# Optimization experiments

Measured on AMD Instinct MI355X. Metric: run time of the kernel, lower is better.

## Reference

```python
import jax, jax.numpy as jnp
import numpy as np

DIM = 256
HEADS = 8
DIM_HEAD = 64
INNER = HEADS * DIM_HEAD  # 512
B, N = 4, 1024


def setup_inputs() -> dict:
    key = jax.random.key(0)
    ks = jax.random.split(key, 7)
    x = jax.random.normal(ks[0], (B, N, DIM), dtype=jnp.float32)
    attn_bias = jax.random.normal(ks[1], (B, HEADS, N, N), dtype=jnp.float32)
    s = 1.0 / np.sqrt(DIM)
    Wq = jax.random.normal(ks[2], (DIM, INNER), dtype=jnp.float32) * s
    Wkv = jax.random.normal(ks[3], (DIM, 2 * INNER), dtype=jnp.float32) * s
    # to_out initialized to zero in the torch module; use small random so output is non-trivial
    Wo = jax.random.normal(ks[4], (INNER, DIM), dtype=jnp.float32) * (1.0 / np.sqrt(INNER))
    bo = jnp.zeros((DIM,), dtype=jnp.float32)
    # gating initialized weight=0, bias=1 -> sigmoid(1); use small random weight + bias 1
    Wg = jax.random.normal(ks[5], (DIM, INNER), dtype=jnp.float32) * 0.02
    bg = jnp.ones((INNER,), dtype=jnp.float32)
    return {"x": x, "attn_bias": attn_bias, "Wq": Wq, "Wkv": Wkv,
            "Wo": Wo, "bo": bo, "Wg": Wg, "bg": bg}


def reference(x, attn_bias, Wq, Wkv, Wo, bo, Wg, bg):
    b, n, _ = x.shape
    scale = DIM_HEAD ** -0.5
    q = x @ Wq                                    # [b, n, inner]
    kv = x @ Wkv                                  # [b, n, 2*inner]
    k, v = jnp.split(kv, 2, axis=-1)
    def split_heads(t):
        return t.reshape(b, n, HEADS, DIM_HEAD).transpose(0, 2, 1, 3)  # [b,h,n,d]
    q, k, v = split_heads(q) * scale, split_heads(k), split_heads(v)
    dots = jnp.einsum('bhid,bhjd->bhij', q, k) + attn_bias
    # explicit max-subtract then softmax (matches original; numerically identical)
    attn = jax.nn.softmax(dots, axis=-1)
    out = jnp.einsum('bhij,bhjd->bhid', attn, v)  # [b,h,n,d]
    out = out.transpose(0, 2, 1, 3).reshape(b, n, INNER)
    gates = jax.nn.sigmoid(x @ Wg + bg)
    out = out * gates
    return out @ Wo + bo
```

## Files before the change

### kernel.cpp

```cpp
#include <hip/hip_runtime.h>

typedef unsigned short u16;
typedef unsigned int u32;
typedef __attribute__((ext_vector_type(8))) __bf16 bf16x8;
typedef __attribute__((ext_vector_type(4))) float floatx4;
typedef const __attribute__((address_space(1))) unsigned char glob_u8;
typedef __attribute__((address_space(3))) unsigned char lds_u8;

#define DEV __device__ __forceinline__

DEV u16 f2bf(float f) {
  return __builtin_bit_cast(u16, (__bf16)f);
}
DEV float bf2f(u16 h) {
  u32 u = ((u32)h) << 16;
  return __builtin_bit_cast(float, u);
}
DEV floatx4 MFMA(bf16x8 a, bf16x8 b, floatx4 c) {
  return __builtin_amdgcn_mfma_f32_16x16x32_bf16(a, b, c, 0, 0, 0);
}

__global__ void convert_k(const float* __restrict__ x, const float* __restrict__ Wq,
                          const float* __restrict__ Wkv, const float* __restrict__ Wg,
                          const float* __restrict__ Wo,
                          u16* __restrict__ xb, u16* __restrict__ WcatT, u16* __restrict__ WoT) {
  int i = blockIdx.x * 256 + threadIdx.x;
  if (i < 1048576) { xb[i] = f2bf(x[i]); return; }
  i -= 1048576;
  if (i < 524288) {
    int n = i >> 8, kk = i & 255;
    float v;
    if (n < 512) v = Wq[kk * 512 + n];
    else if (n < 1536) v = Wkv[kk * 1024 + (n - 512)];
    else v = Wg[kk * 512 + (n - 1536)];
    WcatT[i] = f2bf(v);
    return;
  }
  i -= 524288;
  if (i < 131072) {
    int n = i >> 9, kk = i & 511;
    WoT[i] = f2bf(Wo[kk * 256 + n]);
  }
}

__global__ __launch_bounds__(256, 4) void gemm_qkvg(
    const u16* __restrict__ xb, const u16* __restrict__ WcatT, const float* __restrict__ bg,
    u16* __restrict__ qb, u16* __restrict__ kfrag, u16* __restrict__ vfrag, u16* __restrict__ gb) {
  __shared__ __attribute__((aligned(16))) u16 As[128 * 40];
  __shared__ __attribute__((aligned(16))) u16 Bs[64 * 40];
  const int tid = threadIdx.x;
  const int wave = tid >> 6, lane = tid & 63;
  const int lane15 = lane & 15, quad = lane >> 4;
  const int rm0 = blockIdx.x * 128;
  const int cn0 = blockIdx.y * 64;
  const int wm = (wave & 1) * 64, wn = (wave >> 1) * 32;
  const int rowA = tid >> 1, segA = (tid & 1) * 16;
  const int rowB = tid >> 2, segB = (tid & 3) * 8;
  floatx4 acc[4][2] = {};
  uint4 a0 = *(const uint4*)(xb + (rm0 + rowA) * 256 + segA);
  uint4 a1 = *(const uint4*)(xb + (rm0 + rowA) * 256 + segA + 8);
  uint4 b0 = *(const uint4*)(WcatT + (cn0 + rowB) * 256 + segB);
#pragma unroll 1
  for (int k0 = 0; k0 < 256; k0 += 32) {
    __syncthreads();
    *(uint4*)(As + rowA * 40 + segA) = a0;
    *(uint4*)(As + rowA * 40 + segA + 8) = a1;
    *(uint4*)(Bs + rowB * 40 + segB) = b0;
    __syncthreads();
    if (k0 < 224) {
      a0 = *(const uint4*)(xb + (rm0 + rowA) * 256 + k0 + 32 + segA);
      a1 = *(const uint4*)(xb + (rm0 + rowA) * 256 + k0 + 32 + segA + 8);
      b0 = *(const uint4*)(WcatT + (cn0 + rowB) * 256 + k0 + 32 + segB);
    }
    bf16x8 af[4], bfr[2];
#pragma unroll
    for (int mt = 0; mt < 4; ++mt) af[mt] = *(const bf16x8*)(As + (wm + mt * 16 + lane15) * 40 + quad * 8);
#pragma unroll
    for (int nt = 0; nt < 2; ++nt) bfr[nt] = *(const bf16x8*)(Bs + (wn + nt * 16 + lane15) * 40 + quad * 8);
#pragma unroll
    for (int mt = 0; mt < 4; ++mt)
#pragma unroll
      for (int nt = 0; nt < 2; ++nt)
        acc[mt][nt] = MFMA(af[mt], bfr[nt], acc[mt][nt]);
  }
#pragma unroll
  for (int mt = 0; mt < 4; ++mt)
#pragma unroll
    for (int nt = 0; nt < 2; ++nt)
#pragma unroll
      for (int r = 0; r < 4; ++r) {
        int row = rm0 + wm + mt * 16 + quad * 4 + r;
        int col = cn0 + wn + nt * 16 + lane15;
        float v = acc[mt][nt][r];
        int b = row >> 10, n = row & 1023;
        if (col < 512) {
          int h = col >> 6, d = col & 63;
          qb[((b * 8 + h) * 1024 + n) * 64 + d] = f2bf(v * 0.125f);
        } else if (col < 1024) {
          int c = col - 512, h = c >> 6, d = c & 63;
          int bh2 = b * 8 + h;
          int t = n >> 4, l15 = n & 15;
          int half = d >> 5, qd = (d >> 3) & 3, e = d & 7;
          kfrag[(size_t)bh2 * 65536 + t * 1024 + half * 512 + (qd * 16 + l15) * 8 + e] = f2bf(v);
        } else if (col < 1536) {
          int c = col - 1024, h = c >> 6, d = c & 63;
          int bh2 = b * 8 + h;
          int t64 = n >> 6, ck = (n >> 5) & 1, qd = (n >> 3) & 3, e = n & 7;
          int dt = d >> 4, l15 = d & 15;
          vfrag[(size_t)bh2 * 65536 + t64 * 4096 + dt * 1024 + ck * 512 + (qd * 16 + l15) * 8 + e] = f2bf(v);
        } else {
          int c = col - 1536;
          float g = 1.0f / (1.0f + __expf(-(v + bg[c])));
          gb[row * 512 + c] = f2bf(g);
        }
      }
}

__global__ __launch_bounds__(256, 3) void attn_k(
    const u16* __restrict__ qb, const u16* __restrict__ kfrag, const u16* __restrict__ vfrag,
    const float* __restrict__ bias, const u16* __restrict__ gb, u16* __restrict__ ogb) {
  __shared__ __attribute__((aligned(16))) u16 Kt[2][4096];
  __shared__ __attribute__((aligned(16))) u16 Vt[2][4096];
  __shared__ __attribute__((aligned(16))) u16 Ps[4 * 16 * 72];
  const int tid = threadIdx.x;
  const int wave = tid >> 6, lane = tid & 63;
  const int lane15 = lane & 15, quad = lane >> 4;
  const int bh = blockIdx.x;
  const int q0 = blockIdx.y * 64;

  bf16x8 qf0, qf1;
  {
    const u16* qrow = qb + ((size_t)(bh * 1024 + q0 + wave * 16 + lane15)) * 64 + quad * 8;
    qf0 = *(const bf16x8*)(qrow);
    qf1 = *(const bf16x8*)(qrow + 32);
  }
  bf16x8 ones;
#pragma unroll
  for (int e = 0; e < 8; ++e) ones[e] = __builtin_bit_cast(__bf16, (u16)0x3F80);

  floatx4 oacc[4] = {};
  floatx4 lacc = {};

  u16* Pw = Ps + wave * (16 * 72);
  const u16* kp = kfrag + (size_t)bh * 65536;
  const u16* vp = vfrag + (size_t)bh * 65536;
  const float* bbase = bias + ((size_t)(bh * 1024 + q0 + wave * 16 + quad * 4)) * 1024 + lane15;

  auto stage = [&](int kt, int bufi) {
    const int kb0 = kt * 64;
    const u16* kS = kp + kb0 * 64;
    const u16* vS = vp + kb0 * 64;
#pragma unroll
    for (int c = 0; c < 2; ++c) {
      int ch = wave * 2 + c;
      __builtin_amdgcn_global_load_lds((glob_u8*)(kS + ch * 512 + lane * 8),
                                       (lds_u8*)(&Kt[bufi][ch * 512]), 16, 0, 0);
      __builtin_amdgcn_global_load_lds((glob_u8*)(vS + ch * 512 + lane * 8),
                                       (lds_u8*)(&Vt[bufi][ch * 512]), 16, 0, 0);
    }
  };

  stage(0, 0);
  __syncthreads();
  int cur = 0;
#pragma unroll 1
  for (int kt = 0; kt < 16; ++kt) {
    if (kt < 15) stage(kt + 1, cur ^ 1);
    float bv[4][4];
#pragma unroll
    for (int r = 0; r < 4; ++r)
#pragma unroll
      for (int j = 0; j < 4; ++j)
        bv[r][j] = bbase[r * 1024 + kt * 64 + j * 16];
    const u16* Ktc = Kt[cur];
    const u16* Vtc = Vt[cur];
    floatx4 s[4];
#pragma unroll
    for (int j = 0; j < 4; ++j) {
      bf16x8 kf0 = *(const bf16x8*)(Ktc + j * 1024 + lane * 8);
      bf16x8 kf1 = *(const bf16x8*)(Ktc + j * 1024 + 512 + lane * 8);
      floatx4 z = {};
      z = MFMA(qf0, kf0, z);
      s[j] = MFMA(qf1, kf1, z);
    }
#pragma unroll
    for (int j = 0; j < 4; ++j)
#pragma unroll
      for (int r = 0; r < 4; ++r)
        s[j][r] = __expf(s[j][r] + bv[r][j] - 8.0f);
#pragma unroll
    for (int j = 0; j < 4; ++j)
#pragma unroll
      for (int r = 0; r < 4; ++r)
        Pw[(quad * 4 + r) * 72 + j * 16 + lane15] = f2bf(s[j][r]);
    bf16x8 pf0 = *(const bf16x8*)(Pw + lane15 * 72 + quad * 8);
    bf16x8 pf1 = *(const bf16x8*)(Pw + lane15 * 72 + 32 + quad * 8);

    lacc = MFMA(pf0, ones, lacc);
    lacc = MFMA(pf1, ones, lacc);
#pragma unroll
    for (int dt = 0; dt < 4; ++dt) {
      bf16x8 vf0 = *(const bf16x8*)(Vtc + dt * 1024 + lane * 8);
      bf16x8 vf1 = *(const bf16x8*)(Vtc + dt * 1024 + 512 + lane * 8);
      oacc[dt] = MFMA(pf0, vf0, oacc[dt]);
      oacc[dt] = MFMA(pf1, vf1, oacc[dt]);
    }
    __syncthreads();
    cur ^= 1;
  }

  const int b = bh >> 3, h = bh & 7;
#pragma unroll
  for (int r = 0; r < 4; ++r) {
    int q = q0 + wave * 16 + quad * 4 + r;
    float inv = 1.0f / lacc[r];
    size_t base = ((size_t)(b * 1024 + q)) * 512 + h * 64;
#pragma unroll
    for (int dt = 0; dt < 4; ++dt) {
      size_t gi = base + dt * 16 + lane15;
      ogb[gi] = f2bf(oacc[dt][r] * inv * bf2f(gb[gi]));
    }
  }
}

__global__ __launch_bounds__(256, 4) void gemm_out_k(
    const u16* __restrict__ og, const u16* __restrict__ WoT,
    const float* __restrict__ bo, float* __restrict__ out) {
  __shared__ __attribute__((aligned(16))) u16 As[64 * 40];
  __shared__ __attribute__((aligned(16))) u16 Bs[64 * 40];
  const int tid = threadIdx.x;
  const int wave = tid >> 6, lane = tid & 63;
  const int lane15 = lane & 15, quad = lane >> 4;
  const int rm0 = blockIdx.x * 64;
  const int cn0 = blockIdx.y * 64;
  const int wm = (wave & 1) * 32, wn = (wave >> 1) * 32;
  const int rowA = tid >> 2, segA = (tid & 3) * 8;
  floatx4 acc[2][2] = {};
  uint4 a0 = *(const uint4*)(og + (rm0 + rowA) * 512 + segA);
  uint4 b0 = *(const uint4*)(WoT + (cn0 + rowA) * 512 + segA);
#pragma unroll 1
  for (int k0 = 0; k0 < 512; k0 += 32) {
    __syncthreads();
    *(uint4*)(As + rowA * 40 + segA) = a0;
    *(uint4*)(Bs + rowA * 40 + segA) = b0;
    __syncthreads();
    if (k0 < 480) {
      a0 = *(const uint4*)(og + (rm0 + rowA) * 512 + k0 + 32 + segA);
      b0 = *(const uint4*)(WoT + (cn0 + rowA) * 512 + k0 + 32 + segA);
    }
    bf16x8 af[2], bfr[2];
#pragma unroll
    for (int mt = 0; mt < 2; ++mt) af[mt] = *(const bf16x8*)(As + (wm + mt * 16 + lane15) * 40 + quad * 8);
#pragma unroll
    for (int nt = 0; nt < 2; ++nt) bfr[nt] = *(const bf16x8*)(Bs + (wn + nt * 16 + lane15) * 40 + quad * 8);
#pragma unroll
    for (int mt = 0; mt < 2; ++mt)
#pragma unroll
      for (int nt = 0; nt < 2; ++nt)
        acc[mt][nt] = MFMA(af[mt], bfr[nt], acc[mt][nt]);
  }
#pragma unroll
  for (int nt = 0; nt < 2; ++nt) {
    int col = cn0 + wn + nt * 16 + lane15;
    float bv = bo[col];
#pragma unroll
    for (int mt = 0; mt < 2; ++mt)
#pragma unroll
      for (int r = 0; r < 4; ++r) {
        int row = rm0 + wm + mt * 16 + quad * 4 + r;
        out[(size_t)row * 256 + col] = acc[mt][nt][r] + bv;
      }
  }
}

extern "C" void kernel_launch(void* const* d_in, const int* in_sizes, int n_in,
                              void* d_out, int out_size, void* d_ws, size_t ws_size,
                              hipStream_t stream) {
  const float* x = (const float*)d_in[0];
  const float* bias = (const float*)d_in[1];
  const float* Wq = (const float*)d_in[2];
  const float* Wkv = (const float*)d_in[3];
  const float* Wo = (const float*)d_in[4];
  const float* bo = (const float*)d_in[5];
  const float* Wg = (const float*)d_in[6];
  const float* bg = (const float*)d_in[7];
  float* out = (float*)d_out;
  char* ws = (char*)d_ws;
  u16* xb    = (u16*)(ws);
  u16* WcatT = (u16*)(ws + 2097152);
  u16* WoT   = (u16*)(ws + 3145728);
  u16* qb    = (u16*)(ws + 3407872);
  u16* kfrag = (u16*)(ws + 7602176);
  u16* vfrag = (u16*)(ws + 11796480);
  u16* gb    = (u16*)(ws + 15990784);
  u16* ogb   = (u16*)(ws + 20185088);

  convert_k<<<6656, 256, 0, stream>>>(x, Wq, Wkv, Wg, Wo, xb, WcatT, WoT);
  dim3 g1(32, 32);
  gemm_qkvg<<<g1, 256, 0, stream>>>(xb, WcatT, bg, qb, kfrag, vfrag, gb);
  dim3 g2(32, 16);
  attn_k<<<g2, 256, 0, stream>>>(qb, kfrag, vfrag, bias, gb, ogb);
  dim3 g3(64, 4);
  gemm_out_k<<<g3, 256, 0, stream>>>(ogb, WoT, bo, out);
}
```

Measured before the change: 254.8 us.

## Split attention key tiles across wave pairs with LDS reduction, doubling block count

Each attention block now handles 32 queries instead of 64. Its four waves are split into two query halves times two key halves, and the partial outputs and row sums are combined through LDS at the end. The grid doubles to 1024 blocks, giving more parallelism and occupancy (launch bounds raised to 4) on a kernel dominated by the attention-bias stream. The cost is twice the K/V tile loads from global memory per query and an extra reduction with a barrier.

```diff
diff --git a/kernel.cpp b/kernel.cpp
--- a/kernel.cpp
+++ b/kernel.cpp
@@ -116,21 +116,23 @@
       }
 }
 
-__global__ __launch_bounds__(256, 3) void attn_k(
+__global__ __launch_bounds__(256, 4) void attn_k(
     const u16* __restrict__ qb, const u16* __restrict__ kfrag, const u16* __restrict__ vfrag,
     const float* __restrict__ bias, const u16* __restrict__ gb, u16* __restrict__ ogb) {
   __shared__ __attribute__((aligned(16))) u16 Kt[2][4096];
   __shared__ __attribute__((aligned(16))) u16 Vt[2][4096];
-  __shared__ __attribute__((aligned(16))) u16 Ps[4 * 16 * 72];
+  __shared__ __attribute__((aligned(16))) u16 Ps[4 * 16 * 40];
   const int tid = threadIdx.x;
   const int wave = tid >> 6, lane = tid & 63;
   const int lane15 = lane & 15, quad = lane >> 4;
   const int bh = blockIdx.x;
-  const int q0 = blockIdx.y * 64;
+  const int q0 = blockIdx.y * 32;
+  const int qw = (wave & 1) * 16;
+  const int kh = wave >> 1;
 
   bf16x8 qf0, qf1;
   {
-    const u16* qrow = qb + ((size_t)(bh * 1024 + q0 + wave * 16 + lane15)) * 64 + quad * 8;
+    const u16* qrow = qb + ((size_t)(bh * 1024 + q0 + qw + lane15)) * 64 + quad * 8;
     qf0 = *(const bf16x8*)(qrow);
     qf1 = *(const bf16x8*)(qrow + 32);
   }
@@ -141,15 +143,14 @@
   floatx4 oacc[4] = {};
   floatx4 lacc = {};
 
-  u16* Pw = Ps + wave * (16 * 72);
+  u16* Pw = Ps + wave * (16 * 40);
   const u16* kp = kfrag + (size_t)bh * 65536;
   const u16* vp = vfrag + (size_t)bh * 65536;
-  const float* bbase = bias + ((size_t)(bh * 1024 + q0 + wave * 16 + quad * 4)) * 1024 + lane15;
+  const float* bbase = bias + ((size_t)(bh * 1024 + q0 + qw + quad * 4)) * 1024 + kh * 32 + lane15;
 
   auto stage = [&](int kt, int bufi) {
-    const int kb0 = kt * 64;
-    const u16* kS = kp + kb0 * 64;
-    const u16* vS = vp + kb0 * 64;
+    const u16* kS = kp + kt * 4096;
+    const u16* vS = vp + kt * 4096;
 #pragma unroll
     for (int c = 0; c < 2; ++c) {
       int ch = wave * 2 + c;
@@ -166,59 +167,77 @@
 #pragma unroll 1
   for (int kt = 0; kt < 16; ++kt) {
     if (kt < 15) stage(kt + 1, cur ^ 1);
-    float bv[4][4];
+    float bv[4][2];
 #pragma unroll
     for (int r = 0; r < 4; ++r)
 #pragma unroll
-      for (int j = 0; j < 4; ++j)
+      for (int j = 0; j < 2; ++j)
         bv[r][j] = bbase[r * 1024 + kt * 64 + j * 16];
     const u16* Ktc = Kt[cur];
     const u16* Vtc = Vt[cur];
-    floatx4 s[4];
-#pragma unroll
-    for (int j = 0; j < 4; ++j) {
-      bf16x8 kf0 = *(const bf16x8*)(Ktc + j * 1024 + lane * 8);
-      bf16x8 kf1 = *(const bf16x8*)(Ktc + j * 1024 + 512 + lane * 8);
+    floatx4 s[2];
+#pragma unroll
+    for (int j = 0; j < 2; ++j) {
+      const u16* kb = Ktc + (kh * 2 + j) * 1024 + lane * 8;
+      bf16x8 kf0 = *(const bf16x8*)(kb);
+      bf16x8 kf1 = *(const bf16x8*)(kb + 512);
       floatx4 z = {};
       z = MFMA(qf0, kf0, z);
       s[j] = MFMA(qf1, kf1, z);
     }
 #pragma unroll
-    for (int j = 0; j < 4; ++j)
+    for (int j = 0; j < 2; ++j)
 #pragma unroll
       for (int r = 0; r < 4; ++r)
         s[j][r] = __expf(s[j][r] + bv[r][j] - 8.0f);
 #pragma unroll
-    for (int j = 0; j < 4; ++j)
+    for (int j = 0; j < 2; ++j)
 #pragma unroll
       for (int r = 0; r < 4; ++r)
-        Pw[(quad * 4 + r) * 72 + j * 16 + lane15] = f2bf(s[j][r]);
-    bf16x8 pf0 = *(const bf16x8*)(Pw + lane15 * 72 + quad * 8);
-    bf16x8 pf1 = *(const bf16x8*)(Pw + lane15 * 72 + 32 + quad * 8);
-
-    lacc = MFMA(pf0, ones, lacc);
-    lacc = MFMA(pf1, ones, lacc);
+        Pw[(quad * 4 + r) * 40 + j * 16 + lane15] = f2bf(s[j][r]);
+    bf16x8 pf = *(const bf16x8*)(Pw + lane15 * 40 + quad * 8);
+
+    lacc = MFMA(pf, ones, lacc);
 #pragma unroll
     for (int dt = 0; dt < 4; ++dt) {
-      bf16x8 vf0 = *(const bf16x8*)(Vtc + dt * 1024 + lane * 8);
-      bf16x8 vf1 = *(const bf16x8*)(Vtc + dt * 1024 + 512 + lane * 8);
-      oacc[dt] = MFMA(pf0, vf0, oacc[dt]);
-      oacc[dt] = MFMA(pf1, vf1, oacc[dt]);
+      bf16x8 vf = *(const bf16x8*)(Vtc + dt * 1024 + kh * 512 + lane * 8);
+      oacc[dt] = MFMA(pf, vf, oacc[dt]);
     }
     __syncthreads();
     cur ^= 1;
   }
 
-  const int b = bh >> 3, h = bh & 7;
-#pragma unroll
-  for (int r = 0; r < 4; ++r) {
-    int q = q0 + wave * 16 + quad * 4 + r;
-    float inv = 1.0f / lacc[r];
-    size_t base = ((size_t)(b * 1024 + q)) * 512 + h * 64;
-#pragma unroll
-    for (int dt = 0; dt < 4; ++dt) {
-      size_t gi = base + dt * 16 + lane15;
-      ogb[gi] = f2bf(oacc[dt][r] * inv * bf2f(gb[gi]));
+  float* red = (float*)Kt;
+  if (wave >= 2) {
+    float* r0 = red + (wave - 2) * 1280 + lane * 20;
+#pragma unroll
+    for (int dt = 0; dt < 4; ++dt)
+#pragma unroll
+      for (int r = 0; r < 4; ++r) r0[dt * 4 + r] = oacc[dt][r];
+#pragma unroll
+    for (int r = 0; r < 4; ++r) r0[16 + r] = lacc[r];
+  }
+  __syncthreads();
+  if (wave < 2) {
+    const float* r0 = red + wave * 1280 + lane * 20;
+#pragma unroll
+    for (int dt = 0; dt < 4; ++dt)
+#pragma unroll
+      for (int r = 0; r < 4; ++r) oacc[dt][r] += r0[dt * 4 + r];
+#pragma unroll
+    for (int r = 0; r < 4; ++r) lacc[r] += r0[16 + r];
+
+    const int b = bh >> 3, h = bh & 7;
+#pragma unroll
+    for (int r = 0; r < 4; ++r) {
+      int q = q0 + wave * 16 + quad * 4 + r;
+      float inv = 1.0f / lacc[r];
+      size_t base = ((size_t)(b * 1024 + q)) * 512 + h * 64;
+#pragma unroll
+      for (int dt = 0; dt < 4; ++dt) {
+        size_t gi = base + dt * 16 + lane15;
+        ogb[gi] = f2bf(oacc[dt][r] * inv * bf2f(gb[gi]));
+      }
     }
   }
 }
@@ -298,7 +317,7 @@
   convert_k<<<6656, 256, 0, stream>>>(x, Wq, Wkv, Wg, Wo, xb, WcatT, WoT);
   dim3 g1(32, 32);
   gemm_qkvg<<<g1, 256, 0, stream>>>(xb, WcatT, bg, qb, kfrag, vfrag, gb);
-  dim3 g2(32, 16);
+  dim3 g2(32, 32);
   attn_k<<<g2, 256, 0, stream>>>(qb, kfrag, vfrag, bias, gb, ogb);
   dim3 g3(64, 4);
   gemm_out_k<<<g3, 256, 0, stream>>>(ogb, WoT, bo, out);
```

New measurement: 253.3 us. About the same (-0.6%).
